# Performance work log

Hardware: AMD Instinct MI355X
Metric: run time of the kernel (lower is better)

The kernel has to match this reference:

```python
import jax, jax.numpy as jnp
import numpy as np
from jax import lax

B, N, T, D = 16, 307, 48, 128
H, DK = 8, 16          # nb_head, d_k = d_model // nb_head
K = 3                  # kernel_size
PAD = K - 1
SEGS = (12, 12, 24)    # w_length, d_length, h_length
SCALE = 1.0 / float(np.sqrt(DK))


def _causal_conv_proj(x, w, b):
    """x: (B, N, Ts, D) -> (B, N, H, Ts, DK) via causal Conv2d((1,K)) along time."""
    xc = x.transpose(0, 3, 1, 2)  # (B, D, N, Ts)
    y = lax.conv_general_dilated(
        xc, w, window_strides=(1, 1), padding=[(0, 0), (PAD, PAD)],
        dimension_numbers=("NCHW", "OIHW", "NCHW"))
    y = y[..., :-PAD] + b[None, :, None, None]          # trim right pad -> causal
    b_, _, n_, t_ = y.shape
    # view(B, H, DK, N, Ts).permute(0, 3, 1, 4, 2)
    return y.reshape(b_, H, DK, n_, t_).transpose(0, 3, 1, 4, 2)


def setup_inputs() -> dict:
    rng = jax.random.key(0)
    ks = jax.random.split(rng, 11)
    s = 0.05
    mask = jnp.broadcast_to(jnp.tril(jnp.ones((T, T), jnp.int32)), (B, T, T))
    return {
        "query": jax.random.normal(ks[0], (B, N, T, D), jnp.float32),
        "key": jax.random.normal(ks[1], (B, N, T, D), jnp.float32),
        "value": jax.random.normal(ks[2], (B, N, T, D), jnp.float32),
        "mask": mask,
        "conv_q_w": jax.random.normal(ks[3], (D, D, 1, K), jnp.float32) * s,
        "conv_q_b": jax.random.normal(ks[4], (D,), jnp.float32) * s,
        "conv_k_w": jax.random.normal(ks[5], (D, D, 1, K), jnp.float32) * s,
        "conv_k_b": jax.random.normal(ks[6], (D,), jnp.float32) * s,
        "lin_v_w": jax.random.normal(ks[7], (D, D), jnp.float32) * s,
        "lin_v_b": jax.random.normal(ks[8], (D,), jnp.float32) * s,
        "lin_o_w": jax.random.normal(ks[9], (D, D), jnp.float32) * s,
        "lin_o_b": jax.random.normal(ks[10], (D,), jnp.float32) * s,
    }


def reference(query, key, value, mask,
              conv_q_w, conv_q_b, conv_k_w, conv_k_b,
              lin_v_w, lin_v_b, lin_o_w, lin_o_b):
    # query_multi_segment = key_multi_segment = True: causal conv per time segment
    offs = np.concatenate([[0], np.cumsum(SEGS)])
    q = jnp.concatenate(
        [_causal_conv_proj(query[:, :, offs[i]:offs[i + 1], :], conv_q_w, conv_q_b)
         for i in range(len(SEGS))], axis=3)                    # (B, N, H, T, DK)
    k = jnp.concatenate(
        [_causal_conv_proj(key[:, :, offs[i]:offs[i + 1], :], conv_k_w, conv_k_b)
         for i in range(len(SEGS))], axis=3)                    # (B, N, H, T, DK)
    # value projection: Linear then (B, N, T, H, DK) -> (B, N, H, T, DK)
    v = (jnp.einsum('bntd,ed->bnte', value, lin_v_w) + lin_v_b)
    v = v.reshape(B, N, T, H, DK).transpose(0, 1, 3, 2, 4)
    # masked scaled-dot-product attention
    scores = jnp.einsum('bnhtd,bnhsd->bnhts', q, k) * SCALE     # (B, N, H, T, T)
    scores = jnp.where(mask[:, None, None] == 0, -1e9, scores)
    p = jax.nn.softmax(scores, axis=-1)
    x = jnp.einsum('bnhts,bnhsd->bnhtd', p, v)
    x = x.transpose(0, 1, 3, 2, 4).reshape(B, N, T, H * DK)     # (B, N, T, D)
    return jnp.einsum('bntd,ed->bnte', x, lin_o_w) + lin_o_b
```

## Files before the change

### kernel.cpp

```cpp
#include <hip/hip_runtime.h>
#include <hip/hip_bf16.h>


typedef __attribute__((ext_vector_type(8))) short short8;
typedef __attribute__((ext_vector_type(4))) float floatx4;
typedef __attribute__((ext_vector_type(4))) unsigned short ushortx4;

#define MFMA16(a, b, c) __builtin_amdgcn_mfma_f32_16x16x32_bf16((a), (b), (c), 0, 0, 0)

__device__ __forceinline__ unsigned short f2bf(float x) {
  __hip_bfloat16 h = __float2bfloat16(x);
  return __builtin_bit_cast(unsigned short, h);
}

__device__ __forceinline__ int prow(int t) {
  return t + 2 + (t >= 12 ? 2 : 0) + (t >= 24 ? 2 : 0);
}

__device__ __forceinline__ short8 lds8(const __hip_bfloat16* p) {
  return *(const short8*)p;
}

__global__ void prep_weights(const float* __restrict__ wq,
                             const float* __restrict__ wk,
                             const float* __restrict__ vw,
                             const float* __restrict__ ow,
                             __hip_bfloat16* __restrict__ dst) {
  int i = blockIdx.x * 256 + threadIdx.x;
  float v;
  if (i < 98304) {
    int which = i / 49152;
    int r = i % 49152;
    int tap = r / 16384;
    int rr = r & 16383;
    int e = rr >> 7, d = rr & 127;
    const float* src = which ? wk : wq;
    v = src[e * 384 + d * 3 + tap];
  } else {
    int r = i - 98304;
    int j = r & 16383;
    v = (r >> 14) ? ow[j] : vw[j];
  }
  dst[i] = __float2bfloat16(v);
}

constexpr int XS = 136;
constexpr int QS = 136;
constexpr int VS = 56;
constexpr int WQ_OFF = 0;
constexpr int WK_OFF = 49152;
constexpr int VW_OFF = 98304;
constexpr int OW_OFF = 114688;

__device__ __forceinline__ void stage_tile(const float* __restrict__ src,
                                           __hip_bfloat16* sh_xpad, int tid) {
  const float4* g = (const float4*)src;
  #pragma unroll
  for (int it = 0; it < 6; ++it) {
    int c = tid + it * 256;
    int t = c >> 5;
    int col = (c & 31) * 4;
    float4 f = g[c];
    ushortx4 pk;
    pk[0] = f2bf(f.x); pk[1] = f2bf(f.y); pk[2] = f2bf(f.z); pk[3] = f2bf(f.w);
    *(ushortx4*)&sh_xpad[prow(t) * XS + col] = pk;
  }
}

__device__ __forceinline__ void conv_proj(const __hip_bfloat16* sh_xpad,
                                          const __hip_bfloat16* __restrict__ wt,
                                          const float* __restrict__ bias,
                                          __hip_bfloat16* dst,
                                          int wv, int quad, int l16) {
  const int e0 = (wv * 2) * 16 + l16;
  const int e1 = (wv * 2 + 1) * 16 + l16;
  floatx4 acc[3][2] = {};
  #pragma unroll
  for (int tap = 0; tap < 3; ++tap) {
    const __hip_bfloat16* W = wt + tap * 16384;
    const int sh = 2 - tap;
    #pragma unroll
    for (int ks = 0; ks < 4; ++ks) {
      int k0 = ks * 32 + quad * 8;
      short8 b0 = lds8(W + e0 * 128 + k0);
      short8 b1 = lds8(W + e1 * 128 + k0);
      #pragma unroll
      for (int mi = 0; mi < 3; ++mi) {
        int t = mi * 16 + l16;
        short8 a = lds8(&sh_xpad[(prow(t) - sh) * XS + k0]);
        acc[mi][0] = MFMA16(a, b0, acc[mi][0]);
        acc[mi][1] = MFMA16(a, b1, acc[mi][1]);
      }
    }
  }
  #pragma unroll
  for (int nti = 0; nti < 2; ++nti) {
    int e = (wv * 2 + nti) * 16 + l16;
    float bb = bias[e];
    #pragma unroll
    for (int mi = 0; mi < 3; ++mi) {
      int t0 = mi * 16 + quad * 4;
      #pragma unroll
      for (int r = 0; r < 4; ++r)
        dst[(t0 + r) * QS + e] = __float2bfloat16(acc[mi][nti][r] + bb);
    }
  }
}

__global__ __launch_bounds__(256, 2) void fused_attn(
    const float* __restrict__ gq, const float* __restrict__ gk,
    const float* __restrict__ gv,
    const __hip_bfloat16* __restrict__ wts,
    const float* __restrict__ cqb, const float* __restrict__ ckb,
    const float* __restrict__ vb, const float* __restrict__ ob,
    float* __restrict__ out) {
  __shared__ __align__(16) __hip_bfloat16 sh_xpad[54 * XS];
  __shared__ __align__(16) __hip_bfloat16 sh_q[48 * QS];
  __shared__ __align__(16) __hip_bfloat16 sh_k[48 * QS];
  __shared__ __align__(16) __hip_bfloat16 sh_vt[128 * VS];
  __shared__ __align__(16) __hip_bfloat16 sh_p[4 * 16 * 64];

  const int tid  = threadIdx.x;
  const int wv   = tid >> 6;
  const int lane = tid & 63;
  const int quad = lane >> 4;
  const int l16  = lane & 15;
  const long base = (long)blockIdx.x * (48 * 128);

  const __hip_bfloat16* wq_t = wts + WQ_OFF;
  const __hip_bfloat16* wk_t = wts + WK_OFF;
  const __hip_bfloat16* vw   = wts + VW_OFF;
  const __hip_bfloat16* ow   = wts + OW_OFF;

  if (tid < 102) {
    int pr = tid / 17, pc = tid % 17;
    int row = (pr >> 1) * 14 + (pr & 1);
    uint4 z = {0, 0, 0, 0};
    *(uint4*)&sh_xpad[row * XS + pc * 8] = z;
  }

  stage_tile(gv + base, sh_xpad, tid);
  __syncthreads();

  const int e0 = (wv * 2) * 16 + l16;
  const int e1 = (wv * 2 + 1) * 16 + l16;
  {
    floatx4 acc[3][2] = {};
    #pragma unroll
    for (int ks = 0; ks < 4; ++ks) {
      int k0 = ks * 32 + quad * 8;
      short8 b0 = lds8(vw + e0 * 128 + k0);
      short8 b1 = lds8(vw + e1 * 128 + k0);
      #pragma unroll
      for (int mi = 0; mi < 3; ++mi) {
        int t = mi * 16 + l16;
        short8 a = lds8(&sh_xpad[prow(t) * XS + k0]);
        acc[mi][0] = MFMA16(a, b0, acc[mi][0]);
        acc[mi][1] = MFMA16(a, b1, acc[mi][1]);
      }
    }
    #pragma unroll
    for (int nti = 0; nti < 2; ++nti) {
      int e = (wv * 2 + nti) * 16 + l16;
      float bv = vb[e];
      #pragma unroll
      for (int mi = 0; mi < 3; ++mi) {
        int t0 = mi * 16 + quad * 4;
        ushortx4 pk;
        #pragma unroll
        for (int r = 0; r < 4; ++r) pk[r] = f2bf(acc[mi][nti][r] + bv);
        *(ushortx4*)&sh_vt[e * VS + t0] = pk;
      }
    }
  }
  __syncthreads();

  stage_tile(gq + base, sh_xpad, tid);
  __syncthreads();
  conv_proj(sh_xpad, wq_t, cqb, sh_q, wv, quad, l16);
  __syncthreads();

  stage_tile(gk + base, sh_xpad, tid);
  __syncthreads();
  conv_proj(sh_xpad, wk_t, ckb, sh_k, wv, quad, l16);
  __syncthreads();

  {
    __hip_bfloat16* shp = sh_p + wv * (16 * 64);
    if (lane < 32) {
      int lt = lane >> 1;
      int cp = (6 + (lane & 1)) ^ (lt & 7);
      uint4 z = {0, 0, 0, 0};
      *(uint4*)&shp[lt * 64 + cp * 8] = z;
    }
    short8 zf = {0, 0, 0, 0, 0, 0, 0, 0};
    #pragma unroll
    for (int hi = 0; hi < 2; ++hi) {
      const int hq = (wv * 2 + hi) * 16;
      #pragma unroll
      for (int mi = 0; mi < 3; ++mi) {
        floatx4 s0 = {}, s1 = {}, s2 = {};
        short8 aq  = (quad < 2) ? lds8(&sh_q[(mi * 16 + l16) * QS + hq + quad * 8]) : zf;
        short8 bk0 = (quad < 2) ? lds8(&sh_k[(l16) * QS + hq + quad * 8]) : zf;
        short8 bk1 = (quad < 2) ? lds8(&sh_k[(16 + l16) * QS + hq + quad * 8]) : zf;
        short8 bk2 = (quad < 2) ? lds8(&sh_k[(32 + l16) * QS + hq + quad * 8]) : zf;
        s0 = MFMA16(aq, bk0, s0);
        s1 = MFMA16(aq, bk1, s1);
        s2 = MFMA16(aq, bk2, s2);
        const int tb = mi * 16 + quad * 4;
        #pragma unroll
        for (int r = 0; r < 4; ++r) {
          int t = tb + r;
          float v0 = (l16 <= t)      ? s0[r] * 0.25f : -1e30f;
          float v1 = (16 + l16 <= t) ? s1[r] * 0.25f : -1e30f;
          float v2 = (32 + l16 <= t) ? s2[r] * 0.25f : -1e30f;
          float mx = fmaxf(v0, fmaxf(v1, v2));
          #pragma unroll
          for (int d = 1; d < 16; d <<= 1) mx = fmaxf(mx, __shfl_xor(mx, d, 64));
          float p0 = __expf(v0 - mx), p1 = __expf(v1 - mx), p2 = __expf(v2 - mx);
          float sm = p0 + p1 + p2;
          #pragma unroll
          for (int d = 1; d < 16; d <<= 1) sm += __shfl_xor(sm, d, 64);
          float inv = __builtin_amdgcn_rcpf(sm);
          int lt = quad * 4 + r;
          int xr = lt & 7, lo = l16 & 7, hi8 = l16 >> 3, rowb = lt * 64;
          shp[rowb + (((0 + hi8) ^ xr) << 3) + lo] = __float2bfloat16(p0 * inv);
          shp[rowb + (((2 + hi8) ^ xr) << 3) + lo] = __float2bfloat16(p1 * inv);
          shp[rowb + (((4 + hi8) ^ xr) << 3) + lo] = __float2bfloat16(p2 * inv);
        }
        floatx4 x = {};
        #pragma unroll
        for (int ks = 0; ks < 2; ++ks) {
          int c = (ks * 4 + quad) ^ (l16 & 7);
          short8 ap = lds8(&shp[l16 * 64 + c * 8]);
          int sb = ks * 32 + quad * 8;
          short8 bvv = (sb < 48) ? lds8(&sh_vt[(hq + l16) * VS + sb]) : zf;
          x = MFMA16(ap, bvv, x);
        }
        #pragma unroll
        for (int r = 0; r < 4; ++r)
          sh_xpad[(tb + r) * XS + hq + l16] = __float2bfloat16(x[r]);
      }
    }
  }
  __syncthreads();

  {
    floatx4 acc[3][2] = {};
    #pragma unroll
    for (int ks = 0; ks < 4; ++ks) {
      int k0 = ks * 32 + quad * 8;
      short8 b0 = lds8(ow + e0 * 128 + k0);
      short8 b1 = lds8(ow + e1 * 128 + k0);
      #pragma unroll
      for (int mi = 0; mi < 3; ++mi) {
        short8 a = lds8(&sh_xpad[(mi * 16 + l16) * XS + k0]);
        acc[mi][0] = MFMA16(a, b0, acc[mi][0]);
        acc[mi][1] = MFMA16(a, b1, acc[mi][1]);
      }
    }
    float* op = out + base;
    #pragma unroll
    for (int nti = 0; nti < 2; ++nti) {
      int e = (wv * 2 + nti) * 16 + l16;
      float bo = ob[e];
      #pragma unroll
      for (int mi = 0; mi < 3; ++mi) {
        int t0 = mi * 16 + quad * 4;
        #pragma unroll
        for (int r = 0; r < 4; ++r)
          op[(t0 + r) * 128 + e] = acc[mi][nti][r] + bo;
      }
    }
  }
}

extern "C" void kernel_launch(void* const* d_in, const int* in_sizes, int n_in,
                              void* d_out, int out_size, void* d_ws, size_t ws_size,
                              hipStream_t stream) {
  (void)in_sizes; (void)n_in; (void)out_size; (void)ws_size;
  const float* query = (const float*)d_in[0];
  const float* key   = (const float*)d_in[1];
  const float* value = (const float*)d_in[2];
  const float* cqw = (const float*)d_in[4];
  const float* cqb = (const float*)d_in[5];
  const float* ckw = (const float*)d_in[6];
  const float* ckb = (const float*)d_in[7];
  const float* vw  = (const float*)d_in[8];
  const float* vb  = (const float*)d_in[9];
  const float* ow  = (const float*)d_in[10];
  const float* ob  = (const float*)d_in[11];

  __hip_bfloat16* wts = (__hip_bfloat16*)d_ws;

  prep_weights<<<dim3(512), 256, 0, stream>>>(cqw, ckw, vw, ow, wts);
  fused_attn<<<dim3(16 * 307), 256, 0, stream>>>(
      query, key, value, wts, cqb, ckb, vb, ob, (float*)d_out);
}
```

Baseline: 529.4 us.

## Double-buffer input staging and overlap global loads with projections, raise occupancy

Splits tile staging into a register load and a later LDS write, so the global loads for the next input (q, then k) are in flight while the current projection's MFMAs run. Q and K projection outputs now overwrite the two ping-pong staging buffers in place instead of using separate sh_q/sh_k arrays. This shrinks LDS use, and launch bounds go from 2 to 3 blocks per CU. It also cuts one barrier phase. The cost is more registers held live for the prefetched float4 data under a tighter register budget, with some risk of spills.

```diff
diff --git a/kernel.cpp b/kernel.cpp
--- a/kernel.cpp
+++ b/kernel.cpp
@@ -45,36 +45,39 @@
 }
 
 constexpr int XS = 136;
-constexpr int QS = 136;
 constexpr int VS = 56;
 constexpr int WQ_OFF = 0;
 constexpr int WK_OFF = 49152;
 constexpr int VW_OFF = 98304;
 constexpr int OW_OFF = 114688;
 
-__device__ __forceinline__ void stage_tile(const float* __restrict__ src,
-                                           __hip_bfloat16* sh_xpad, int tid) {
+__device__ __forceinline__ void stage_load(const float* __restrict__ src,
+                                           float4* r, int tid) {
   const float4* g = (const float4*)src;
+  #pragma unroll
+  for (int it = 0; it < 6; ++it) r[it] = g[tid + it * 256];
+}
+
+__device__ __forceinline__ void stage_write(const float4* r,
+                                            __hip_bfloat16* sh, int tid) {
   #pragma unroll
   for (int it = 0; it < 6; ++it) {
     int c = tid + it * 256;
     int t = c >> 5;
     int col = (c & 31) * 4;
-    float4 f = g[c];
+    float4 f = r[it];
     ushortx4 pk;
     pk[0] = f2bf(f.x); pk[1] = f2bf(f.y); pk[2] = f2bf(f.z); pk[3] = f2bf(f.w);
-    *(ushortx4*)&sh_xpad[prow(t) * XS + col] = pk;
-  }
-}
-
-__device__ __forceinline__ void conv_proj(const __hip_bfloat16* sh_xpad,
-                                          const __hip_bfloat16* __restrict__ wt,
-                                          const float* __restrict__ bias,
-                                          __hip_bfloat16* dst,
-                                          int wv, int quad, int l16) {
+    *(ushortx4*)&sh[prow(t) * XS + col] = pk;
+  }
+}
+
+__device__ __forceinline__ void conv_acc(const __hip_bfloat16* shx,
+                                         const __hip_bfloat16* __restrict__ wt,
+                                         floatx4 acc[3][2],
+                                         int wv, int quad, int l16) {
   const int e0 = (wv * 2) * 16 + l16;
   const int e1 = (wv * 2 + 1) * 16 + l16;
-  floatx4 acc[3][2] = {};
   #pragma unroll
   for (int tap = 0; tap < 3; ++tap) {
     const __hip_bfloat16* W = wt + tap * 16384;
@@ -87,12 +90,18 @@
       #pragma unroll
       for (int mi = 0; mi < 3; ++mi) {
         int t = mi * 16 + l16;
-        short8 a = lds8(&sh_xpad[(prow(t) - sh) * XS + k0]);
+        short8 a = lds8(&shx[(prow(t) - sh) * XS + k0]);
         acc[mi][0] = MFMA16(a, b0, acc[mi][0]);
         acc[mi][1] = MFMA16(a, b1, acc[mi][1]);
       }
     }
   }
+}
+
+__device__ __forceinline__ void conv_write(floatx4 acc[3][2],
+                                           const float* __restrict__ bias,
+                                           __hip_bfloat16* dst,
+                                           int wv, int quad, int l16) {
   #pragma unroll
   for (int nti = 0; nti < 2; ++nti) {
     int e = (wv * 2 + nti) * 16 + l16;
@@ -102,21 +111,20 @@
       int t0 = mi * 16 + quad * 4;
       #pragma unroll
       for (int r = 0; r < 4; ++r)
-        dst[(t0 + r) * QS + e] = __float2bfloat16(acc[mi][nti][r] + bb);
-    }
-  }
-}
-
-__global__ __launch_bounds__(256, 2) void fused_attn(
+        dst[(t0 + r) * XS + e] = __float2bfloat16(acc[mi][nti][r] + bb);
+    }
+  }
+}
+
+__global__ __launch_bounds__(256, 3) void fused_attn(
     const float* __restrict__ gq, const float* __restrict__ gk,
     const float* __restrict__ gv,
     const __hip_bfloat16* __restrict__ wts,
     const float* __restrict__ cqb, const float* __restrict__ ckb,
     const float* __restrict__ vb, const float* __restrict__ ob,
     float* __restrict__ out) {
-  __shared__ __align__(16) __hip_bfloat16 sh_xpad[54 * XS];
-  __shared__ __align__(16) __hip_bfloat16 sh_q[48 * QS];
-  __shared__ __align__(16) __hip_bfloat16 sh_k[48 * QS];
+  __shared__ __align__(16) __hip_bfloat16 shA[54 * XS];
+  __shared__ __align__(16) __hip_bfloat16 shB[54 * XS];
   __shared__ __align__(16) __hip_bfloat16 sh_vt[128 * VS];
   __shared__ __align__(16) __hip_bfloat16 sh_p[4 * 16 * 64];
 
@@ -132,57 +140,71 @@
   const __hip_bfloat16* vw   = wts + VW_OFF;
   const __hip_bfloat16* ow   = wts + OW_OFF;
 
-  if (tid < 102) {
-    int pr = tid / 17, pc = tid % 17;
+  if (tid < 204) {
+    int b = tid >= 102;
+    int i = b ? tid - 102 : tid;
+    int pr = i / 17, pc = i % 17;
     int row = (pr >> 1) * 14 + (pr & 1);
     uint4 z = {0, 0, 0, 0};
-    *(uint4*)&sh_xpad[row * XS + pc * 8] = z;
-  }
-
-  stage_tile(gv + base, sh_xpad, tid);
-  __syncthreads();
+    __hip_bfloat16* s = b ? shB : shA;
+    *(uint4*)&s[row * XS + pc * 8] = z;
+  }
 
   const int e0 = (wv * 2) * 16 + l16;
   const int e1 = (wv * 2 + 1) * 16 + l16;
-  {
-    floatx4 acc[3][2] = {};
-    #pragma unroll
-    for (int ks = 0; ks < 4; ++ks) {
-      int k0 = ks * 32 + quad * 8;
-      short8 b0 = lds8(vw + e0 * 128 + k0);
-      short8 b1 = lds8(vw + e1 * 128 + k0);
-      #pragma unroll
-      for (int mi = 0; mi < 3; ++mi) {
-        int t = mi * 16 + l16;
-        short8 a = lds8(&sh_xpad[prow(t) * XS + k0]);
-        acc[mi][0] = MFMA16(a, b0, acc[mi][0]);
-        acc[mi][1] = MFMA16(a, b1, acc[mi][1]);
-      }
-    }
-    #pragma unroll
-    for (int nti = 0; nti < 2; ++nti) {
-      int e = (wv * 2 + nti) * 16 + l16;
-      float bv = vb[e];
-      #pragma unroll
-      for (int mi = 0; mi < 3; ++mi) {
-        int t0 = mi * 16 + quad * 4;
-        ushortx4 pk;
-        #pragma unroll
-        for (int r = 0; r < 4; ++r) pk[r] = f2bf(acc[mi][nti][r] + bv);
-        *(ushortx4*)&sh_vt[e * VS + t0] = pk;
-      }
-    }
-  }
-  __syncthreads();
-
-  stage_tile(gq + base, sh_xpad, tid);
-  __syncthreads();
-  conv_proj(sh_xpad, wq_t, cqb, sh_q, wv, quad, l16);
-  __syncthreads();
-
-  stage_tile(gk + base, sh_xpad, tid);
-  __syncthreads();
-  conv_proj(sh_xpad, wk_t, ckb, sh_k, wv, quad, l16);
+
+  float4 rv[6];
+  stage_load(gv + base, rv, tid);
+  stage_write(rv, shA, tid);
+  float4 rq[6];
+  stage_load(gq + base, rq, tid);
+  __syncthreads();
+
+  floatx4 vacc[3][2] = {};
+  #pragma unroll
+  for (int ks = 0; ks < 4; ++ks) {
+    int k0 = ks * 32 + quad * 8;
+    short8 b0 = lds8(vw + e0 * 128 + k0);
+    short8 b1 = lds8(vw + e1 * 128 + k0);
+    #pragma unroll
+    for (int mi = 0; mi < 3; ++mi) {
+      int t = mi * 16 + l16;
+      short8 a = lds8(&shA[prow(t) * XS + k0]);
+      vacc[mi][0] = MFMA16(a, b0, vacc[mi][0]);
+      vacc[mi][1] = MFMA16(a, b1, vacc[mi][1]);
+    }
+  }
+  stage_write(rq, shB, tid);
+  float4 rk[6];
+  stage_load(gk + base, rk, tid);
+  __syncthreads();
+
+  #pragma unroll
+  for (int nti = 0; nti < 2; ++nti) {
+    int e = (wv * 2 + nti) * 16 + l16;
+    float bv = vb[e];
+    #pragma unroll
+    for (int mi = 0; mi < 3; ++mi) {
+      int t0 = mi * 16 + quad * 4;
+      ushortx4 pk;
+      #pragma unroll
+      for (int r = 0; r < 4; ++r) pk[r] = f2bf(vacc[mi][nti][r] + bv);
+      *(ushortx4*)&sh_vt[e * VS + t0] = pk;
+    }
+  }
+
+  floatx4 qacc[3][2] = {};
+  conv_acc(shB, wq_t, qacc, wv, quad, l16);
+  stage_write(rk, shA, tid);
+  __syncthreads();
+
+  conv_write(qacc, cqb, shB, wv, quad, l16);
+
+  floatx4 kacc[3][2] = {};
+  conv_acc(shA, wk_t, kacc, wv, quad, l16);
+  __syncthreads();
+
+  conv_write(kacc, ckb, shA, wv, quad, l16);
   __syncthreads();
 
   {
@@ -200,10 +222,10 @@
       #pragma unroll
       for (int mi = 0; mi < 3; ++mi) {
         floatx4 s0 = {}, s1 = {}, s2 = {};
-        short8 aq  = (quad < 2) ? lds8(&sh_q[(mi * 16 + l16) * QS + hq + quad * 8]) : zf;
-        short8 bk0 = (quad < 2) ? lds8(&sh_k[(l16) * QS + hq + quad * 8]) : zf;
-        short8 bk1 = (quad < 2) ? lds8(&sh_k[(16 + l16) * QS + hq + quad * 8]) : zf;
-        short8 bk2 = (quad < 2) ? lds8(&sh_k[(32 + l16) * QS + hq + quad * 8]) : zf;
+        short8 aq  = (quad < 2) ? lds8(&shB[(mi * 16 + l16) * XS + hq + quad * 8]) : zf;
+        short8 bk0 = (quad < 2) ? lds8(&shA[(l16) * XS + hq + quad * 8]) : zf;
+        short8 bk1 = (quad < 2) ? lds8(&shA[(16 + l16) * XS + hq + quad * 8]) : zf;
+        short8 bk2 = (quad < 2) ? lds8(&shA[(32 + l16) * XS + hq + quad * 8]) : zf;
         s0 = MFMA16(aq, bk0, s0);
         s1 = MFMA16(aq, bk1, s1);
         s2 = MFMA16(aq, bk2, s2);
@@ -239,7 +261,7 @@
         }
         #pragma unroll
         for (int r = 0; r < 4; ++r)
-          sh_xpad[(tb + r) * XS + hq + l16] = __float2bfloat16(x[r]);
+          shB[(tb + r) * XS + hq + l16] = __float2bfloat16(x[r]);
       }
     }
   }
@@ -254,7 +276,7 @@
       short8 b1 = lds8(ow + e1 * 128 + k0);
       #pragma unroll
       for (int mi = 0; mi < 3; ++mi) {
-        short8 a = lds8(&sh_xpad[(mi * 16 + l16) * XS + k0]);
+        short8 a = lds8(&shB[(mi * 16 + l16) * XS + k0]);
         acc[mi][0] = MFMA16(a, b0, acc[mi][0]);
         acc[mi][1] = MFMA16(a, b1, acc[mi][1]);
       }
```

Result: faster. 484.3 us (-8.5%).
